# Kernel tuning notes

Measured on AMD Instinct MI355X. Metric: run time of the kernel, lower is better.

Reference implementation:

```python
import jax, jax.numpy as jnp
import numpy as np

K = 5       # kernel_size
NV = 12     # number of orientation vectors
CIN = 8
COUT = 8

ICO = np.array([[-0.525731, 0.850651, 0.0], [0.525731, 0.850651, 0.0],
                [-0.525731, -0.850651, 0.0], [0.525731, -0.850651, 0.0],
                [0.0, -0.525731, 0.850651], [0.0, 0.525731, 0.850651],
                [0.0, -0.525731, -0.850651], [0.0, 0.525731, -0.850651],
                [0.850651, 0.0, -0.525731], [0.850651, 0.0, 0.525731],
                [-0.850651, 0.0, -0.525731], [-0.850651, 0.0, 0.525731]],
               dtype=np.float32)


def _attrs():
    # invariant_attr_r3s2_fiber_bundle on the fixed k^3 stencil graph
    off = np.arange(K) - K // 2 + (K + 1) % 2 * 0.5
    grid = np.stack(np.meshgrid(off, off, off, indexing='ij'), 0)
    pos = grid.transpose(1, 2, 3, 0).reshape(-1, 3)              # [K^3, 3]
    rel = pos[K ** 3 // 2][None, :] - pos                        # pos_send - pos_receive, [E,3]
    inv1 = (rel[:, None, :] * ICO[None]).sum(-1, keepdims=True)  # [E,NV,1] parallel component
    inv2 = np.linalg.norm(rel[:, None, :] - inv1 * ICO[None], axis=-1, keepdims=True)  # orthogonal norm
    spatial = np.concatenate([inv1, inv2], -1).round(5).reshape(-1, 2)   # rounded as in module
    spherical = (ICO @ ICO.T).round(3).reshape(-1, 1)                     # [NV*NV, 1]
    return jnp.asarray(spatial, jnp.float32), jnp.asarray(spherical, jnp.float32)


def _poly(x, degree=3):
    # PolynomialFeatures: cat of x, x(x)x, x(x)x(x)x flattened
    feats = [x]
    for _ in range(1, degree):
        f = feats[-1][..., :, None] * x[..., None, :]
        feats.append(f.reshape(f.shape[:-2] + (-1,)))
    return jnp.concatenate(feats, -1)


def _mlp(a, w1, b1, w2, b2, w3):
    h = jax.nn.gelu(a @ w1.T + b1, approximate=False)
    h = jax.nn.gelu(h @ w2.T + b2, approximate=False)
    return h @ w3.T


def setup_inputs() -> dict:
    key = jax.random.key(0)
    ks = jax.random.split(key, 8)
    spatial, spherical = _attrs()

    def lin(k, o, i):
        return (jax.random.normal(k, (o, i), jnp.float32) / np.sqrt(i)).astype(jnp.float32)

    return dict(
        x=jax.random.normal(ks[0], (2, CIN, NV, 64, 64, 64), jnp.float32),
        spatial_attr=spatial,            # [1500, 2]
        spherical_attr=spherical,        # [144, 1]
        basis_w1=lin(ks[1], 8, 14), basis_b1=jnp.zeros(8, jnp.float32),
        basis_w2=lin(ks[2], 8, 8),  basis_b2=jnp.zeros(8, jnp.float32),
        basis_w3=lin(ks[3], CIN, 8),
        fiber_w1=lin(ks[4], 8, 3),  fiber_b1=jnp.zeros(8, jnp.float32),
        fiber_w2=lin(ks[5], 8, 8),  fiber_b2=jnp.zeros(8, jnp.float32),
        fiber_w3=lin(ks[6], CIN * COUT, 8),
        bias=jnp.full((1, COUT, 1, 1, 1, 1), 0.01, jnp.float32),
    )


def reference(x, spatial_attr, spherical_attr,
              basis_w1, basis_b1, basis_w2, basis_b2, basis_w3,
              fiber_w1, fiber_b1, fiber_w2, fiber_b2, fiber_w3, bias):
    # Spatial (depthwise) kernel generated by tiny MLP on edge invariants.
    # (Original uniques attrs then gathers; basis(unique)[inverse] == basis(attr), so apply directly.)
    sw = _mlp(_poly(spatial_attr), basis_w1, basis_b1, basis_w2, basis_b2, basis_w3)  # [K^3*NV, CIN]
    sw = sw.reshape(K, K, K, NV, CIN).transpose(4, 3, 0, 1, 2).reshape(CIN * NV, 1, K, K, K)
    # Fiber (orientation-mixing) weights from MLP on orientation invariants.
    fw = _mlp(_poly(spherical_attr), fiber_w1, fiber_b1, fiber_w2, fiber_b2, fiber_w3)  # [NV*NV, CIN*COUT]
    fw = fw.reshape(NV, NV, CIN, COUT).transpose(3, 2, 0, 1)  # [COUT, CIN, NV, NV]

    B, _, _, X, Y, Z = x.shape
    xr = x.reshape(B, CIN * NV, X, Y, Z)
    y = jax.lax.conv_general_dilated(
        xr, sw, window_strides=(1, 1, 1), padding='SAME',
        feature_group_count=CIN * NV,
        dimension_numbers=('NCDHW', 'OIDHW', 'NCDHW'))
    y = y.reshape(B, CIN, NV, X, Y, Z)
    out = jnp.einsum('bfvxyz,gfvw->bgwxyz', y, fw)
    return out + bias
```

## Files before the change

### kernel.cpp

```cpp
#include <hip/hip_runtime.h>
#include <math.h>

#define DEV __device__ __forceinline__

DEV float gelu_exact(float v) {
    return 0.5f * v * (1.0f + erff(v * 0.7071067811865476f));
}

typedef __attribute__((ext_vector_type(8))) short bf16x8;
typedef __attribute__((ext_vector_type(4))) float f32x4;

DEV short f2b(float f) {
    unsigned u = __builtin_bit_cast(unsigned, f);
    unsigned r = (u + 0x7fffu + ((u >> 16) & 1u)) >> 16;
    return (short)r;
}

__global__ __launch_bounds__(256) void wk(
    const float* __restrict__ spatial, const float* __restrict__ spherical,
    const float* __restrict__ bw1, const float* __restrict__ bb1,
    const float* __restrict__ bw2, const float* __restrict__ bb2,
    const float* __restrict__ bw3,
    const float* __restrict__ fw1, const float* __restrict__ fb1,
    const float* __restrict__ fw2, const float* __restrict__ fb2,
    const float* __restrict__ fw3,
    float* __restrict__ sw, unsigned short* __restrict__ Mtt) {
    const int i = blockIdx.x * 256 + threadIdx.x;
    if (i < 1500) {
        const float a = spatial[2 * i], b = spatial[2 * i + 1];
        float ft[14];
        ft[0] = a; ft[1] = b;
        ft[2] = a * a; ft[3] = a * b; ft[4] = b * a; ft[5] = b * b;
#pragma unroll
        for (int k = 0; k < 4; ++k) {
            ft[6 + 2 * k] = ft[2 + k] * a;
            ft[7 + 2 * k] = ft[2 + k] * b;
        }
        float h1[8], h2[8];
#pragma unroll
        for (int j = 0; j < 8; ++j) {
            float s = bb1[j];
#pragma unroll
            for (int k = 0; k < 14; ++k) s = fmaf(bw1[j * 14 + k], ft[k], s);
            h1[j] = gelu_exact(s);
        }
#pragma unroll
        for (int j = 0; j < 8; ++j) {
            float s = bb2[j];
#pragma unroll
            for (int k = 0; k < 8; ++k) s = fmaf(bw2[j * 8 + k], h1[k], s);
            h2[j] = gelu_exact(s);
        }
        const int o = i / 12, v = i % 12;
#pragma unroll
        for (int c = 0; c < 8; ++c) {
            float s = 0.f;
#pragma unroll
            for (int k = 0; k < 8; ++k) s = fmaf(bw3[c * 8 + k], h2[k], s);
            sw[(c * 12 + v) * 125 + o] = s;
        }
    } else if (i < 1644) {
        const int r = i - 1500;
        const float s0 = spherical[r];
        float ft[3];
        ft[0] = s0; ft[1] = s0 * s0; ft[2] = s0 * s0 * s0;
        float h1[8], h2[8];
#pragma unroll
        for (int j = 0; j < 8; ++j) {
            float s = fb1[j];
#pragma unroll
            for (int k = 0; k < 3; ++k) s = fmaf(fw1[j * 3 + k], ft[k], s);
            h1[j] = gelu_exact(s);
        }
#pragma unroll
        for (int j = 0; j < 8; ++j) {
            float s = fb2[j];
#pragma unroll
            for (int k = 0; k < 8; ++k) s = fmaf(fw2[j * 8 + k], h1[k], s);
            h2[j] = gelu_exact(s);
        }
        const int v = r / 12, w = r % 12;
#pragma unroll
        for (int c = 0; c < 64; ++c) {
            float s = 0.f;
#pragma unroll
            for (int k = 0; k < 8; ++k) s = fmaf(fw3[c * 8 + k], h2[k], s);
            const int f = c >> 3, g = c & 7;
            Mtt[(g * 12 + w) * 96 + f * 12 + v] = (unsigned short)f2b(s);
        }
    }
}

#define CPITCH 80
__global__ __launch_bounds__(256) void ck(const float* __restrict__ x,
                                          const float* __restrict__ sw,
                                          float* __restrict__ y) {
    __shared__ float lds[12 * 12 * CPITCH];
    const int ch = blockIdx.y, b = blockIdx.z;
    const int ty = (blockIdx.x & 7) << 3;
    const int tz = (blockIdx.x >> 3) << 3;
    const int t = threadIdx.x;
    const long cb = (long)(b * 96 + ch) << 18;
    const float* __restrict__ xb = x + cb;
    float* __restrict__ yb = y + cb;
    const float* __restrict__ w = sw + ch * 125;

    {
        const int l16 = t & 15;
        const int rq = t >> 4;
#pragma unroll
        for (int pass = 0; pass < 9; ++pass) {
            const int r = rq + (pass << 4);
            const int zi = r / 12, yi = r % 12;
            const int zz = tz + zi - 2, yy = ty + yi - 2;
            float4 v = {0.f, 0.f, 0.f, 0.f};
            if (zz >= 0 && zz < 64 && yy >= 0 && yy < 64)
                v = *(const float4*)(xb + (zz << 12) + (yy << 6) + (l16 << 2));
            const int s = (r >> 2) & 3;
            float* rp = lds + r * CPITCH;
            float* p0 = rp + (((l16 ^ s) << 2) + 2);
            p0[0] = v.x; p0[1] = v.y;
            float* p1 = rp + (((l16 + 1) ^ s) << 2);
            p1[0] = v.z; p1[1] = v.w;
            if (l16 == 0) {
                float* p = rp + ((0 ^ s) << 2);
                p[0] = 0.f; p[1] = 0.f;
            }
            if (l16 == 15) {
                float* p = rp + (((16 ^ s) << 2) + 2);
                p[0] = 0.f; p[1] = 0.f;
            }
        }
    }
    __syncthreads();

    const int xg = t & 7;
    const int yg = (t >> 3) & 3;
    const int zg = t >> 5;
    const int w0 = xg << 1;

    float acc[2][8];
#pragma unroll
    for (int i = 0; i < 2; ++i)
#pragma unroll
        for (int j = 0; j < 8; ++j) acc[i][j] = 0.f;

#pragma unroll
    for (int hz = 0; hz < 5; ++hz) {
#pragma unroll
        for (int hy = 0; hy < 6; ++hy) {
            const int row = (zg + hz) * 12 + (yg << 1) + hy;
            const int s = (row >> 2) & 3;
            const float* rp = lds + row * CPITCH;
            const float4 fa = *(const float4*)(rp + (((w0 + 0) ^ s) << 2));
            const float4 fb = *(const float4*)(rp + (((w0 + 1) ^ s) << 2));
            const float4 fc = *(const float4*)(rp + (((w0 + 2) ^ s) << 2));
            const float f[12] = {fa.x, fa.y, fa.z, fa.w, fb.x, fb.y, fb.z, fb.w,
                                 fc.x, fc.y, fc.z, fc.w};
#pragma unroll
            for (int dy = 0; dy < 2; ++dy) {
                const int B = hy - dy;
                if (B < 0 || B > 4) continue;
                const float* wr = w + (hz * 5 + B) * 5;
#pragma unroll
                for (int C = 0; C < 5; ++C) {
                    const float wv = wr[C];
#pragma unroll
                    for (int dx = 0; dx < 8; ++dx)
                        acc[dy][dx] = fmaf(f[C + dx], wv, acc[dy][dx]);
                }
            }
        }
    }

    const int zo = tz + zg;
    const int xo = xg << 3;
#pragma unroll
    for (int dy = 0; dy < 2; ++dy) {
        const int yo = ty + (yg << 1) + dy;
        float* op = yb + (zo << 12) + (yo << 6) + xo;
        float4 o0 = {acc[dy][0], acc[dy][1], acc[dy][2], acc[dy][3]};
        float4 o1 = {acc[dy][4], acc[dy][5], acc[dy][6], acc[dy][7]};
        *(float4*)(op) = o0;
        *(float4*)(op + 4) = o1;
    }
}

#define EPITCH 132
__global__ __launch_bounds__(256) void ek(float* __restrict__ io,
                                          const unsigned short* __restrict__ Mtt,
                                          const float* __restrict__ bias) {
    __shared__ float yt[96 * EPITCH];
    const int t = threadIdx.x;
    const long b_off = ((long)blockIdx.y * 96) << 18;
    const int pt0 = blockIdx.x << 7;

    {
        const int l32 = t & 31;
        const int r8 = t >> 5;
#pragma unroll
        for (int pass = 0; pass < 12; ++pass) {
            const int fv = r8 + (pass << 3);
            const float4 v = *(const float4*)(io + b_off + ((long)fv << 18) + pt0 + (l32 << 2));
            *(float4*)(yt + fv * EPITCH + (l32 << 2)) = v;
        }
    }
    __syncthreads();

    const int lane = t & 63;
    const int wv = t >> 6;
    const int l15 = lane & 15, quad = lane >> 4;
    const int ptl = wv << 5;

    bf16x8 Bf[2][3];
#pragma unroll
    for (int nt = 0; nt < 2; ++nt)
#pragma unroll
        for (int ks = 0; ks < 3; ++ks)
#pragma unroll
            for (int j = 0; j < 8; ++j) {
                const int fv = ks * 32 + quad * 8 + j;
                Bf[nt][ks][j] = f2b(yt[fv * EPITCH + ptl + nt * 16 + l15]);
            }

    const long po = b_off + pt0 + ptl;
#pragma unroll
    for (int mt = 0; mt < 6; ++mt) {
        bf16x8 Af[3];
#pragma unroll
        for (int ks = 0; ks < 3; ++ks)
            Af[ks] = *(const bf16x8*)(Mtt + (mt * 16 + l15) * 96 + ks * 32 + quad * 8);
#pragma unroll
        for (int nt = 0; nt < 2; ++nt) {
            f32x4 c = {0.f, 0.f, 0.f, 0.f};
#pragma unroll
            for (int ks = 0; ks < 3; ++ks)
                c = __builtin_amdgcn_mfma_f32_16x16x32_bf16(Af[ks], Bf[nt][ks], c, 0, 0, 0);
#pragma unroll
            for (int r = 0; r < 4; ++r) {
                const int gw = mt * 16 + quad * 4 + r;
                io[po + ((long)gw << 18) + nt * 16 + l15] = c[r] + bias[gw / 12];
            }
        }
    }
}

extern "C" void kernel_launch(void* const* d_in, const int* in_sizes, int n_in,
                              void* d_out, int out_size, void* d_ws, size_t ws_size,
                              hipStream_t stream) {
    const float* x        = (const float*)d_in[0];
    const float* spatial  = (const float*)d_in[1];
    const float* spherical= (const float*)d_in[2];
    const float* bw1 = (const float*)d_in[3];
    const float* bb1 = (const float*)d_in[4];
    const float* bw2 = (const float*)d_in[5];
    const float* bb2 = (const float*)d_in[6];
    const float* bw3 = (const float*)d_in[7];
    const float* fw1 = (const float*)d_in[8];
    const float* fb1 = (const float*)d_in[9];
    const float* fw2 = (const float*)d_in[10];
    const float* fb2 = (const float*)d_in[11];
    const float* fw3 = (const float*)d_in[12];
    const float* bias = (const float*)d_in[13];

    float* sw = (float*)d_ws;
    unsigned short* Mtt = (unsigned short*)((char*)d_ws + 48128);
    float* out = (float*)d_out;

    hipLaunchKernelGGL(wk, dim3(7), dim3(256), 0, stream,
                       spatial, spherical, bw1, bb1, bw2, bb2, bw3,
                       fw1, fb1, fw2, fb2, fw3, sw, Mtt);
    hipLaunchKernelGGL(ck, dim3(64, 96, 2), dim3(256), 0, stream, x, sw, out);
    hipLaunchKernelGGL(ek, dim3(2048, 2, 1), dim3(256), 0, stream, out, Mtt, bias);
    (void)in_sizes; (void)n_in; (void)out_size; (void)ws_size;
}
```

Measured before the change: 587.1 us.

## Stage MFMA results through LDS for coalesced float4 stores and re-swizzle LDS layouts

The channel-mixing kernel now writes its MFMA accumulators into a rotated-swizzle LDS tile and then stores them to global memory as coalesced float4 rows with bias added, instead of scattered scalar stores. Its input staging tile drops the padded pitch in favour of a rotation swizzle, so B-fragment reads avoid bank conflicts. The depthwise conv kernel replaces the XOR swizzle with a smaller padded pitch and precomputed row pointers to cut address arithmetic. The cost is an extra LDS round trip and two more barriers in the mixing kernel.

```diff
diff --git a/kernel.cpp b/kernel.cpp
--- a/kernel.cpp
+++ b/kernel.cpp
@@ -91,11 +91,12 @@
     }
 }
 
-#define CPITCH 80
+#define CPITCH 76
+#define WOFF(wn) ((((wn) << 2) + (((wn) >> 3) << 2)))
 __global__ __launch_bounds__(256) void ck(const float* __restrict__ x,
                                           const float* __restrict__ sw,
                                           float* __restrict__ y) {
-    __shared__ float lds[12 * 12 * CPITCH];
+    __shared__ float lds[144 * CPITCH];
     const int ch = blockIdx.y, b = blockIdx.z;
     const int ty = (blockIdx.x & 7) << 3;
     const int tz = (blockIdx.x >> 3) << 3;
@@ -108,6 +109,8 @@
     {
         const int l16 = t & 15;
         const int rq = t >> 4;
+        const int o1 = (l16 << 2) + 2 + ((l16 >> 3) << 2);
+        const int o2 = (l16 << 2) + 4 + ((((l16 + 1) >> 3)) << 2);
 #pragma unroll
         for (int pass = 0; pass < 9; ++pass) {
             const int r = rq + (pass << 4);
@@ -116,20 +119,11 @@
             float4 v = {0.f, 0.f, 0.f, 0.f};
             if (zz >= 0 && zz < 64 && yy >= 0 && yy < 64)
                 v = *(const float4*)(xb + (zz << 12) + (yy << 6) + (l16 << 2));
-            const int s = (r >> 2) & 3;
             float* rp = lds + r * CPITCH;
-            float* p0 = rp + (((l16 ^ s) << 2) + 2);
-            p0[0] = v.x; p0[1] = v.y;
-            float* p1 = rp + (((l16 + 1) ^ s) << 2);
-            p1[0] = v.z; p1[1] = v.w;
-            if (l16 == 0) {
-                float* p = rp + ((0 ^ s) << 2);
-                p[0] = 0.f; p[1] = 0.f;
-            }
-            if (l16 == 15) {
-                float* p = rp + (((16 ^ s) << 2) + 2);
-                p[0] = 0.f; p[1] = 0.f;
-            }
+            rp[o1] = v.x; rp[o1 + 1] = v.y;
+            rp[o2] = v.z; rp[o2 + 1] = v.w;
+            if (l16 == 0)  { rp[0] = 0.f;  rp[1] = 0.f; }
+            if (l16 == 15) { rp[74] = 0.f; rp[75] = 0.f; }
         }
     }
     __syncthreads();
@@ -137,7 +131,10 @@
     const int xg = t & 7;
     const int yg = (t >> 3) & 3;
     const int zg = t >> 5;
-    const int w0 = xg << 1;
+    const int rb = (zg * 12 + (yg << 1)) * CPITCH;
+    const float* p0 = lds + rb + WOFF(2 * xg);
+    const float* p1 = lds + rb + WOFF(2 * xg + 1);
+    const float* p2 = lds + rb + WOFF(2 * xg + 2);
 
     float acc[2][8];
 #pragma unroll
@@ -149,13 +146,11 @@
     for (int hz = 0; hz < 5; ++hz) {
 #pragma unroll
         for (int hy = 0; hy < 6; ++hy) {
-            const int row = (zg + hz) * 12 + (yg << 1) + hy;
-            const int s = (row >> 2) & 3;
-            const float* rp = lds + row * CPITCH;
-            const float4 fa = *(const float4*)(rp + (((w0 + 0) ^ s) << 2));
-            const float4 fb = *(const float4*)(rp + (((w0 + 1) ^ s) << 2));
-            const float4 fc = *(const float4*)(rp + (((w0 + 2) ^ s) << 2));
-            const float f[12] = {fa.x, fa.y, fa.z, fa.w, fb.x, fb.y, fb.z, fb.w,
+            const int ro = (hz * 12 + hy) * CPITCH;
+            const float4 fa = *(const float4*)(p0 + ro);
+            const float4 fb4 = *(const float4*)(p1 + ro);
+            const float4 fc = *(const float4*)(p2 + ro);
+            const float f[12] = {fa.x, fa.y, fa.z, fa.w, fb4.x, fb4.y, fb4.z, fb4.w,
                                  fc.x, fc.y, fc.z, fc.w};
 #pragma unroll
             for (int dy = 0; dy < 2; ++dy) {
@@ -186,11 +181,10 @@
     }
 }
 
-#define EPITCH 132
 __global__ __launch_bounds__(256) void ek(float* __restrict__ io,
                                           const unsigned short* __restrict__ Mtt,
                                           const float* __restrict__ bias) {
-    __shared__ float yt[96 * EPITCH];
+    __shared__ float yt[96 * 128];
     const int t = threadIdx.x;
     const long b_off = ((long)blockIdx.y * 96) << 18;
     const int pt0 = blockIdx.x << 7;
@@ -202,7 +196,8 @@
         for (int pass = 0; pass < 12; ++pass) {
             const int fv = r8 + (pass << 3);
             const float4 v = *(const float4*)(io + b_off + ((long)fv << 18) + pt0 + (l32 << 2));
-            *(float4*)(yt + fv * EPITCH + (l32 << 2)) = v;
+            const int ws = (l32 + ((fv >> 3) << 2)) & 31;
+            *(float4*)(yt + (fv << 7) + (ws << 2)) = v;
         }
     }
     __syncthreads();
@@ -216,14 +211,17 @@
 #pragma unroll
     for (int nt = 0; nt < 2; ++nt)
 #pragma unroll
-        for (int ks = 0; ks < 3; ++ks)
-#pragma unroll
-            for (int j = 0; j < 8; ++j) {
-                const int fv = ks * 32 + quad * 8 + j;
-                Bf[nt][ks][j] = f2b(yt[fv * EPITCH + ptl + nt * 16 + l15]);
-            }
-
-    const long po = b_off + pt0 + ptl;
+        for (int ks = 0; ks < 3; ++ks) {
+            const int pt = ptl + nt * 16 + l15;
+            const int rot = ((ks << 2) + quad) << 2;
+            const int ws = ((pt >> 2) + rot) & 31;
+            const int base = ((ks * 32 + quad * 8) << 7) + (ws << 2) + (pt & 3);
+#pragma unroll
+            for (int j = 0; j < 8; ++j)
+                Bf[nt][ks][j] = f2b(yt[base + (j << 7)]);
+        }
+
+    float cv[6][2][4];
 #pragma unroll
     for (int mt = 0; mt < 6; ++mt) {
         bf16x8 Af[3];
@@ -237,10 +235,38 @@
             for (int ks = 0; ks < 3; ++ks)
                 c = __builtin_amdgcn_mfma_f32_16x16x32_bf16(Af[ks], Bf[nt][ks], c, 0, 0, 0);
 #pragma unroll
-            for (int r = 0; r < 4; ++r) {
-                const int gw = mt * 16 + quad * 4 + r;
-                io[po + ((long)gw << 18) + nt * 16 + l15] = c[r] + bias[gw / 12];
-            }
+            for (int r = 0; r < 4; ++r) cv[mt][nt][r] = c[r];
+        }
+    }
+    __syncthreads();
+
+#pragma unroll
+    for (int mt = 0; mt < 6; ++mt) {
+        const int rot = (((mt << 1) + (quad >> 1))) << 2;
+        const int gw0 = mt * 16 + quad * 4;
+#pragma unroll
+        for (int nt = 0; nt < 2; ++nt) {
+            const int pt = ptl + nt * 16 + l15;
+            const int ws = ((pt >> 2) + rot) & 31;
+            const int base = (gw0 << 7) + (ws << 2) + (pt & 3);
+#pragma unroll
+            for (int r = 0; r < 4; ++r)
+                yt[base + (r << 7)] = cv[mt][nt][r];
+        }
+    }
+    __syncthreads();
+
+    {
+        const int wl = t & 31;
+        const int r8 = t >> 5;
+#pragma unroll
+        for (int pass = 0; pass < 12; ++pass) {
+            const int row = r8 + (pass << 3);
+            const int ws = (wl + (pass << 2)) & 31;
+            float4 v = *(const float4*)(yt + (row << 7) + (ws << 2));
+            const float bs = bias[row / 12];
+            v.x += bs; v.y += bs; v.z += bs; v.w += bs;
+            *(float4*)(io + b_off + ((long)row << 18) + pt0 + (wl << 2)) = v;
         }
     }
 }
```

New measurement: 585.2 us. No clear change (-0.3%).
